# Kernel tuning notes

Measured on AMD Instinct MI355X. Metric: run time of the kernel, lower is better.

## Reference

```python
import jax, jax.numpy as jnp
import numpy as np

TAU = 0.95
MARGIN = 1.0
NUM_NEG = 1

B, S = 4096, 4096
N_RERANK = 8192


def setup_inputs() -> dict:
    key = jax.random.key(0)
    k1, k2, k3 = jax.random.split(key, 3)
    rerank_y = jax.random.normal(k1, (N_RERANK, 1), dtype=jnp.float32)
    # probabilities in (0,1]; keep away from 0 since the loss takes log
    cut_y = jax.random.uniform(k2, (B, S, 1), dtype=jnp.float32, minval=1e-4, maxval=1.0)
    rerank_label = jnp.ones((B, 1), dtype=jnp.float32)  # unused (overwritten by ones in source)
    cut_label = jax.random.randint(k3, (B, S), 0, 2, dtype=jnp.int32)
    return {"rerank_y": rerank_y, "cut_y": cut_y, "rerank_label": rerank_label, "cut_label": cut_label}


def _f1_weights(cut_label):
    # Vectorized Metric_for_Loss.f1(labels[i], j): F1 at cut depth j+1.
    lab = cut_label.astype(jnp.float32)                      # [B,S]
    cum = jnp.cumsum(lab, axis=1)                            # relevant docs within top j+1
    k = jnp.arange(1, lab.shape[1] + 1, dtype=jnp.float32)   # cut depth
    total = jnp.sum(lab, axis=1, keepdims=True)              # total relevant per list
    prec = cum / k
    rec = jnp.where(total > 0, cum / jnp.maximum(total, 1.0), 0.0)
    den = prec + rec
    return jnp.where(den > 0, 2.0 * prec * rec / den, 0.0)   # [B,S]


def _attncut_loss(cut_y, cut_label):
    out2d = jnp.squeeze(cut_y, axis=2)                       # [B,S]
    r = _f1_weights(cut_label)
    # Faithful to source: q = exp(r/tau) is summed into norm_factor, then q := 1/norm_factor
    norm = jnp.sum(jnp.exp(r / TAU), axis=1, keepdims=True)  # [B,1]
    q = 1.0 / norm
    loss_mat = jnp.log(out2d) * q
    return -jnp.sum(loss_mat) / out2d.shape[0]


def _rerank_loss(rerank_y):
    y_pos = rerank_y[:: NUM_NEG + 1, :]                      # [B,1]
    y_neg = rerank_y[1 :: NUM_NEG + 1, :]                    # [B,1] (num_neg=1 -> cat of one)
    y_neg = jnp.mean(y_neg, axis=-1, keepdims=True)
    # margin_ranking_loss with y=1, reduction='mean'
    return jnp.mean(jnp.maximum(0.0, -(y_pos - y_neg) + MARGIN))


def reference(rerank_y, cut_y, rerank_label, cut_label):
    return _attncut_loss(cut_y, cut_label) + _rerank_loss(rerank_y)
```

## Files before the change

### kernel.cpp

```cpp
#include <hip/hip_runtime.h>

#define NROWS 4096
#define NCOLS 4096
#define TAU 0.95f
#define MARGIN 1.0f

__global__ __launch_bounds__(256) void attncut_kernel(
    const float* __restrict__ cut_y, const int* __restrict__ cut_label,
    float* __restrict__ partials) {
  const int row = blockIdx.x;
  const int t = threadIdx.x;
  const int lane = t & 63;
  const int wid = t >> 6;

  const int4* lab4 = (const int4*)(cut_label + (size_t)row * NCOLS) + t * 4;
  const float4* yy4 = (const float4*)(cut_y + (size_t)row * NCOLS) + t * 4;

  const int4 L0 = lab4[0], L1 = lab4[1], L2 = lab4[2], L3 = lab4[3];
  const float4 Y0 = yy4[0], Y1 = yy4[1], Y2 = yy4[2], Y3 = yy4[3];

  const int lsum = L0.x + L0.y + L0.z + L0.w + L1.x + L1.y + L1.z + L1.w +
                   L2.x + L2.y + L2.z + L2.w + L3.x + L3.y + L3.z + L3.w;

  int x = lsum;
#pragma unroll
  for (int off = 1; off < 64; off <<= 1) {
    int v = __shfl_up(x, off, 64);
    if (lane >= off) x += v;
  }
  __shared__ int wsum[4];
  if (lane == 63) wsum[wid] = x;
  __syncthreads();
  int prev = 0;
#pragma unroll
  for (int w = 0; w < 4; ++w)
    if (w < wid) prev += wsum[w];
  const int Ttot = wsum[0] + wsum[1] + wsum[2] + wsum[3];
  int c = prev + x - lsum;

  const float Tf = (float)Ttot;
  const float kbase = (float)(t * 16);
  float norm_acc = 0.f, log_acc = 0.f;

#define STEP(LAB, YV, J)                                           \
  {                                                                \
    c += (LAB);                                                    \
    const float kk = kbase + (float)((J) + 1);                     \
    const float r =                                                \
        (c > 0) ? __fdividef(2.0f * (float)c, kk + Tf) : 0.0f;     \
    norm_acc += __expf(r * (1.0f / TAU));                          \
    log_acc += __logf(YV);                                         \
  }

  STEP(L0.x, Y0.x, 0)  STEP(L0.y, Y0.y, 1)  STEP(L0.z, Y0.z, 2)  STEP(L0.w, Y0.w, 3)
  STEP(L1.x, Y1.x, 4)  STEP(L1.y, Y1.y, 5)  STEP(L1.z, Y1.z, 6)  STEP(L1.w, Y1.w, 7)
  STEP(L2.x, Y2.x, 8)  STEP(L2.y, Y2.y, 9)  STEP(L2.z, Y2.z, 10) STEP(L2.w, Y2.w, 11)
  STEP(L3.x, Y3.x, 12) STEP(L3.y, Y3.y, 13) STEP(L3.z, Y3.z, 14) STEP(L3.w, Y3.w, 15)
#undef STEP

#pragma unroll
  for (int off = 32; off > 0; off >>= 1) {
    norm_acc += __shfl_down(norm_acc, off, 64);
    log_acc += __shfl_down(log_acc, off, 64);
  }
  __shared__ float nred[4], lred[4];
  if (lane == 0) {
    nred[wid] = norm_acc;
    lred[wid] = log_acc;
  }
  __syncthreads();
  if (t == 0) {
    const float norm = nred[0] + nred[1] + nred[2] + nred[3];
    const float ls = lred[0] + lred[1] + lred[2] + lred[3];
    partials[row] = -ls / (norm * (float)NROWS);
  }
}

__global__ __launch_bounds__(256) void finish_kernel(
    const float* __restrict__ partials, const float* __restrict__ rerank_y,
    float* __restrict__ out) {
  const int t = threadIdx.x;
  const int lane = t & 63, wid = t >> 6;

  float acc = 0.f;
  const float4* p4 = (const float4*)partials;
#pragma unroll
  for (int i = 0; i < 4; ++i) {
    float4 v = p4[t + 256 * i];
    acc += (v.x + v.y) + (v.z + v.w);
  }

  float racc = 0.f;
  const float4* y4 = (const float4*)rerank_y;
#pragma unroll
  for (int i = 0; i < 8; ++i) {
    float4 v = y4[t + 256 * i];
    racc += fmaxf(0.f, MARGIN - (v.x - v.y));
    racc += fmaxf(0.f, MARGIN - (v.z - v.w));
  }
  acc += racc * (1.0f / 4096.0f);

#pragma unroll
  for (int off = 32; off > 0; off >>= 1) acc += __shfl_down(acc, off, 64);
  __shared__ float ws[4];
  if (lane == 0) ws[wid] = acc;
  __syncthreads();
  if (t == 0) out[0] = (ws[0] + ws[1]) + (ws[2] + ws[3]);
}

extern "C" void kernel_launch(void* const* d_in, const int* in_sizes, int n_in,
                              void* d_out, int out_size, void* d_ws, size_t ws_size,
                              hipStream_t stream) {
  const float* rerank_y = (const float*)d_in[0];
  const float* cut_y = (const float*)d_in[1];
  const int* cut_label = (const int*)d_in[3];
  float* out = (float*)d_out;
  float* partials = (float*)d_ws;

  attncut_kernel<<<NROWS, 256, 0, stream>>>(cut_y, cut_label, partials);
  finish_kernel<<<1, 256, 0, stream>>>(partials, rerank_y, out);
}
```

Before: 151.2 us.

## Assign one wavefront per row with bit-packed labels and shuffle-only reductions

Result: slower. 166.8 us (+10.3%).

```diff
diff --git a/kernel.cpp b/kernel.cpp
--- a/kernel.cpp
+++ b/kernel.cpp
@@ -5,75 +5,87 @@
 #define TAU 0.95f
 #define MARGIN 1.0f
 
-__global__ __launch_bounds__(256) void attncut_kernel(
+__global__ __launch_bounds__(256, 4) void attncut_kernel(
     const float* __restrict__ cut_y, const int* __restrict__ cut_label,
     float* __restrict__ partials) {
-  const int row = blockIdx.x;
-  const int t = threadIdx.x;
-  const int lane = t & 63;
-  const int wid = t >> 6;
+  const int wid = threadIdx.x >> 6;
+  const int lane = threadIdx.x & 63;
+  const int row = blockIdx.x * 4 + wid;
 
-  const int4* lab4 = (const int4*)(cut_label + (size_t)row * NCOLS) + t * 4;
-  const float4* yy4 = (const float4*)(cut_y + (size_t)row * NCOLS) + t * 4;
+  const int* lbase = cut_label + (size_t)row * NCOLS + lane * 64;
+  const float* ybase = cut_y + (size_t)row * NCOLS + lane * 64;
+  const int4* Lp = (const int4*)lbase;
+  const float4* Yp = (const float4*)ybase;
 
-  const int4 L0 = lab4[0], L1 = lab4[1], L2 = lab4[2], L3 = lab4[3];
-  const float4 Y0 = yy4[0], Y1 = yy4[1], Y2 = yy4[2], Y3 = yy4[3];
+#define LDL(K) const int4 l##K = Lp[K];
+  LDL(0) LDL(1) LDL(2) LDL(3) LDL(4) LDL(5) LDL(6) LDL(7)
+  LDL(8) LDL(9) LDL(10) LDL(11) LDL(12) LDL(13) LDL(14) LDL(15)
+#undef LDL
 
-  const int lsum = L0.x + L0.y + L0.z + L0.w + L1.x + L1.y + L1.z + L1.w +
-                   L2.x + L2.y + L2.z + L2.w + L3.x + L3.y + L3.z + L3.w;
+  unsigned int mlo = 0u, mhi = 0u;
+#define PACKLO(K)                                                          \
+  mlo |= ((unsigned)l##K.x | ((unsigned)l##K.y << 1) |                     \
+          ((unsigned)l##K.z << 2) | ((unsigned)l##K.w << 3))               \
+         << (4 * (K));
+#define PACKHI(K)                                                          \
+  mhi |= ((unsigned)l##K.x | ((unsigned)l##K.y << 1) |                     \
+          ((unsigned)l##K.z << 2) | ((unsigned)l##K.w << 3))               \
+         << (4 * ((K)-8));
+  PACKLO(0) PACKLO(1) PACKLO(2) PACKLO(3)
+  PACKLO(4) PACKLO(5) PACKLO(6) PACKLO(7)
+  PACKHI(8) PACKHI(9) PACKHI(10) PACKHI(11)
+  PACKHI(12) PACKHI(13) PACKHI(14) PACKHI(15)
+#undef PACKLO
+#undef PACKHI
 
-  int x = lsum;
+  const int cnt = __popc(mlo) + __popc(mhi);
+
+  int x = cnt;
 #pragma unroll
   for (int off = 1; off < 64; off <<= 1) {
     int v = __shfl_up(x, off, 64);
     if (lane >= off) x += v;
   }
-  __shared__ int wsum[4];
-  if (lane == 63) wsum[wid] = x;
-  __syncthreads();
-  int prev = 0;
-#pragma unroll
-  for (int w = 0; w < 4; ++w)
-    if (w < wid) prev += wsum[w];
-  const int Ttot = wsum[0] + wsum[1] + wsum[2] + wsum[3];
-  int c = prev + x - lsum;
+  const int Ttot = __shfl(x, 63, 64);
+  int c = x - cnt;
+
+#define LDY(K) const float4 y##K = Yp[K];
+  LDY(0) LDY(1) LDY(2) LDY(3) LDY(4) LDY(5) LDY(6) LDY(7)
+  LDY(8) LDY(9) LDY(10) LDY(11) LDY(12) LDY(13) LDY(14) LDY(15)
+#undef LDY
 
   const float Tf = (float)Ttot;
-  const float kbase = (float)(t * 16);
+  const float kbase = (float)(lane * 64);
   float norm_acc = 0.f, log_acc = 0.f;
 
-#define STEP(LAB, YV, J)                                           \
-  {                                                                \
-    c += (LAB);                                                    \
-    const float kk = kbase + (float)((J) + 1);                     \
-    const float r =                                                \
-        (c > 0) ? __fdividef(2.0f * (float)c, kk + Tf) : 0.0f;     \
-    norm_acc += __expf(r * (1.0f / TAU));                          \
-    log_acc += __logf(YV);                                         \
+#define ELEM(YV, J)                                                        \
+  {                                                                        \
+    const unsigned bit =                                                   \
+        (((J) < 32) ? (mlo >> (J)) : (mhi >> ((J)-32))) & 1u;              \
+    c += (int)bit;                                                         \
+    float r = __fdividef(2.0f * (float)c, kbase + (float)((J) + 1) + Tf);  \
+    r = (c > 0) ? r : 0.0f;                                                \
+    norm_acc += __expf(r * (1.0f / TAU));                                  \
+    log_acc += __logf(YV);                                                 \
   }
-
-  STEP(L0.x, Y0.x, 0)  STEP(L0.y, Y0.y, 1)  STEP(L0.z, Y0.z, 2)  STEP(L0.w, Y0.w, 3)
-  STEP(L1.x, Y1.x, 4)  STEP(L1.y, Y1.y, 5)  STEP(L1.z, Y1.z, 6)  STEP(L1.w, Y1.w, 7)
-  STEP(L2.x, Y2.x, 8)  STEP(L2.y, Y2.y, 9)  STEP(L2.z, Y2.z, 10) STEP(L2.w, Y2.w, 11)
-  STEP(L3.x, Y3.x, 12) STEP(L3.y, Y3.y, 13) STEP(L3.z, Y3.z, 14) STEP(L3.w, Y3.w, 15)
-#undef STEP
+#define ELEM4(K)                                                           \
+  ELEM(y##K.x, 4 * (K) + 0)                                                \
+  ELEM(y##K.y, 4 * (K) + 1)                                                \
+  ELEM(y##K.z, 4 * (K) + 2)                                                \
+  ELEM(y##K.w, 4 * (K) + 3)
+  ELEM4(0) ELEM4(1) ELEM4(2) ELEM4(3)
+  ELEM4(4) ELEM4(5) ELEM4(6) ELEM4(7)
+  ELEM4(8) ELEM4(9) ELEM4(10) ELEM4(11)
+  ELEM4(12) ELEM4(13) ELEM4(14) ELEM4(15)
+#undef ELEM4
+#undef ELEM
 
 #pragma unroll
   for (int off = 32; off > 0; off >>= 1) {
     norm_acc += __shfl_down(norm_acc, off, 64);
     log_acc += __shfl_down(log_acc, off, 64);
   }
-  __shared__ float nred[4], lred[4];
-  if (lane == 0) {
-    nred[wid] = norm_acc;
-    lred[wid] = log_acc;
-  }
-  __syncthreads();
-  if (t == 0) {
-    const float norm = nred[0] + nred[1] + nred[2] + nred[3];
-    const float ls = lred[0] + lred[1] + lred[2] + lred[3];
-    partials[row] = -ls / (norm * (float)NROWS);
-  }
+  if (lane == 0) partials[row] = -log_acc / (norm_acc * (float)NROWS);
 }
 
 __global__ __launch_bounds__(256) void finish_kernel(
@@ -117,6 +129,6 @@
   float* out = (float*)d_out;
   float* partials = (float*)d_ws;
 
-  attncut_kernel<<<NROWS, 256, 0, stream>>>(cut_y, cut_label, partials);
+  attncut_kernel<<<NROWS / 4, 256, 0, stream>>>(cut_y, cut_label, partials);
   finish_kernel<<<1, 256, 0, stream>>>(partials, rerank_y, out);
 }
```

## Split log-sum and F1 norm into separate blocks with coalesced y loads

Applied to the files above, without the earlier changes.

Measured after the change: 154.9 us. 1.02x slower.

```diff
diff --git a/kernel.cpp b/kernel.cpp
--- a/kernel.cpp
+++ b/kernel.cpp
@@ -5,96 +5,103 @@
 #define TAU 0.95f
 #define MARGIN 1.0f
 
-__global__ __launch_bounds__(256) void attncut_kernel(
+__global__ __launch_bounds__(256) void fused_kernel(
     const float* __restrict__ cut_y, const int* __restrict__ cut_label,
-    float* __restrict__ partials) {
-  const int row = blockIdx.x;
+    float* __restrict__ norm_out, float* __restrict__ logsum_out) {
   const int t = threadIdx.x;
   const int lane = t & 63;
   const int wid = t >> 6;
+  __shared__ float red[4];
+  __shared__ int wsum[4];
 
-  const int4* lab4 = (const int4*)(cut_label + (size_t)row * NCOLS) + t * 4;
-  const float4* yy4 = (const float4*)(cut_y + (size_t)row * NCOLS) + t * 4;
+  if (blockIdx.x < NROWS) {
+    const int row = blockIdx.x;
+    const float4* Yp = (const float4*)(cut_y + (size_t)row * NCOLS);
+    const float4 a0 = Yp[t];
+    const float4 a1 = Yp[t + 256];
+    const float4 a2 = Yp[t + 512];
+    const float4 a3 = Yp[t + 768];
+    float s = __logf(a0.x) + __logf(a0.y) + __logf(a0.z) + __logf(a0.w) +
+              __logf(a1.x) + __logf(a1.y) + __logf(a1.z) + __logf(a1.w) +
+              __logf(a2.x) + __logf(a2.y) + __logf(a2.z) + __logf(a2.w) +
+              __logf(a3.x) + __logf(a3.y) + __logf(a3.z) + __logf(a3.w);
+#pragma unroll
+    for (int off = 32; off > 0; off >>= 1) s += __shfl_down(s, off, 64);
+    if (lane == 0) red[wid] = s;
+    __syncthreads();
+    if (t == 0) logsum_out[row] = (red[0] + red[1]) + (red[2] + red[3]);
+  } else {
+    const int row = blockIdx.x - NROWS;
+    const int4* Lp = (const int4*)(cut_label + (size_t)row * NCOLS) + t * 4;
+    const int4 L0 = Lp[0], L1 = Lp[1], L2 = Lp[2], L3 = Lp[3];
 
-  const int4 L0 = lab4[0], L1 = lab4[1], L2 = lab4[2], L3 = lab4[3];
-  const float4 Y0 = yy4[0], Y1 = yy4[1], Y2 = yy4[2], Y3 = yy4[3];
+    const int lsum = L0.x + L0.y + L0.z + L0.w + L1.x + L1.y + L1.z + L1.w +
+                     L2.x + L2.y + L2.z + L2.w + L3.x + L3.y + L3.z + L3.w;
 
-  const int lsum = L0.x + L0.y + L0.z + L0.w + L1.x + L1.y + L1.z + L1.w +
-                   L2.x + L2.y + L2.z + L2.w + L3.x + L3.y + L3.z + L3.w;
+    int x = lsum;
+#pragma unroll
+    for (int off = 1; off < 64; off <<= 1) {
+      int v = __shfl_up(x, off, 64);
+      if (lane >= off) x += v;
+    }
+    if (lane == 63) wsum[wid] = x;
+    __syncthreads();
+    int prev = 0;
+#pragma unroll
+    for (int w = 0; w < 4; ++w)
+      if (w < wid) prev += wsum[w];
+    const int Ttot = wsum[0] + wsum[1] + wsum[2] + wsum[3];
+    int c = prev + x - lsum;
 
-  int x = lsum;
-#pragma unroll
-  for (int off = 1; off < 64; off <<= 1) {
-    int v = __shfl_up(x, off, 64);
-    if (lane >= off) x += v;
+    const float Tf = (float)Ttot;
+    const float kbase = (float)(t * 16);
+    float norm_acc = 0.f;
+
+#define STEP(LAB, J)                                                     \
+  {                                                                      \
+    c += (LAB);                                                          \
+    float r = __fdividef(2.0f * (float)c, kbase + (float)((J) + 1) + Tf);\
+    r = (c > 0) ? r : 0.0f;                                              \
+    norm_acc += __expf(r * (1.0f / TAU));                                \
   }
-  __shared__ int wsum[4];
-  if (lane == 63) wsum[wid] = x;
-  __syncthreads();
-  int prev = 0;
-#pragma unroll
-  for (int w = 0; w < 4; ++w)
-    if (w < wid) prev += wsum[w];
-  const int Ttot = wsum[0] + wsum[1] + wsum[2] + wsum[3];
-  int c = prev + x - lsum;
-
-  const float Tf = (float)Ttot;
-  const float kbase = (float)(t * 16);
-  float norm_acc = 0.f, log_acc = 0.f;
-
-#define STEP(LAB, YV, J)                                           \
-  {                                                                \
-    c += (LAB);                                                    \
-    const float kk = kbase + (float)((J) + 1);                     \
-    const float r =                                                \
-        (c > 0) ? __fdividef(2.0f * (float)c, kk + Tf) : 0.0f;     \
-    norm_acc += __expf(r * (1.0f / TAU));                          \
-    log_acc += __logf(YV);                                         \
-  }
-
-  STEP(L0.x, Y0.x, 0)  STEP(L0.y, Y0.y, 1)  STEP(L0.z, Y0.z, 2)  STEP(L0.w, Y0.w, 3)
-  STEP(L1.x, Y1.x, 4)  STEP(L1.y, Y1.y, 5)  STEP(L1.z, Y1.z, 6)  STEP(L1.w, Y1.w, 7)
-  STEP(L2.x, Y2.x, 8)  STEP(L2.y, Y2.y, 9)  STEP(L2.z, Y2.z, 10) STEP(L2.w, Y2.w, 11)
-  STEP(L3.x, Y3.x, 12) STEP(L3.y, Y3.y, 13) STEP(L3.z, Y3.z, 14) STEP(L3.w, Y3.w, 15)
+    STEP(L0.x, 0)  STEP(L0.y, 1)  STEP(L0.z, 2)  STEP(L0.w, 3)
+    STEP(L1.x, 4)  STEP(L1.y, 5)  STEP(L1.z, 6)  STEP(L1.w, 7)
+    STEP(L2.x, 8)  STEP(L2.y, 9)  STEP(L2.z, 10) STEP(L2.w, 11)
+    STEP(L3.x, 12) STEP(L3.y, 13) STEP(L3.z, 14) STEP(L3.w, 15)
 #undef STEP
 
 #pragma unroll
-  for (int off = 32; off > 0; off >>= 1) {
-    norm_acc += __shfl_down(norm_acc, off, 64);
-    log_acc += __shfl_down(log_acc, off, 64);
-  }
-  __shared__ float nred[4], lred[4];
-  if (lane == 0) {
-    nred[wid] = norm_acc;
-    lred[wid] = log_acc;
-  }
-  __syncthreads();
-  if (t == 0) {
-    const float norm = nred[0] + nred[1] + nred[2] + nred[3];
-    const float ls = lred[0] + lred[1] + lred[2] + lred[3];
-    partials[row] = -ls / (norm * (float)NROWS);
+    for (int off = 32; off > 0; off >>= 1)
+      norm_acc += __shfl_down(norm_acc, off, 64);
+    if (lane == 0) red[wid] = norm_acc;
+    __syncthreads();
+    if (t == 0) norm_out[row] = (red[0] + red[1]) + (red[2] + red[3]);
   }
 }
 
 __global__ __launch_bounds__(256) void finish_kernel(
-    const float* __restrict__ partials, const float* __restrict__ rerank_y,
-    float* __restrict__ out) {
+    const float* __restrict__ norms, const float* __restrict__ logsums,
+    const float* __restrict__ rerank_y, float* __restrict__ out) {
   const int t = threadIdx.x;
   const int lane = t & 63, wid = t >> 6;
 
   float acc = 0.f;
-  const float4* p4 = (const float4*)partials;
+  const float4* n4 = (const float4*)norms;
+  const float4* l4 = (const float4*)logsums;
 #pragma unroll
   for (int i = 0; i < 4; ++i) {
-    float4 v = p4[t + 256 * i];
-    acc += (v.x + v.y) + (v.z + v.w);
+    const float4 n = n4[t + 256 * i];
+    const float4 l = l4[t + 256 * i];
+    acc += __fdividef(l.x, n.x) + __fdividef(l.y, n.y) +
+           __fdividef(l.z, n.z) + __fdividef(l.w, n.w);
   }
+  acc *= -(1.0f / (float)NROWS);
 
   float racc = 0.f;
   const float4* y4 = (const float4*)rerank_y;
 #pragma unroll
   for (int i = 0; i < 8; ++i) {
-    float4 v = y4[t + 256 * i];
+    const float4 v = y4[t + 256 * i];
     racc += fmaxf(0.f, MARGIN - (v.x - v.y));
     racc += fmaxf(0.f, MARGIN - (v.z - v.w));
   }
@@ -115,8 +122,9 @@
   const float* cut_y = (const float*)d_in[1];
   const int* cut_label = (const int*)d_in[3];
   float* out = (float*)d_out;
-  float* partials = (float*)d_ws;
+  float* norms = (float*)d_ws;
+  float* logsums = (float*)d_ws + NROWS;
 
-  attncut_kernel<<<NROWS, 256, 0, stream>>>(cut_y, cut_label, partials);
-  finish_kernel<<<1, 256, 0, stream>>>(partials, rerank_y, out);
+  fused_kernel<<<2 * NROWS, 256, 0, stream>>>(cut_y, cut_label, norms, logsums);
+  finish_kernel<<<1, 256, 0, stream>>>(norms, logsums, rerank_y, out);
 }
```
